# Optimization experiments

Measured on AMD Instinct MI355X. Metric: run time of the kernel, lower is better.

The kernel has to match this reference:

```python
import jax, jax.numpy as jnp
import numpy as np

# --- constants from init_kwargs / module defaults ---
H, W, C = 720, 1280, 2
T_EVT, T_PROP = 10, 10
T_TOTAL = T_EVT + T_PROP          # 20 temporal steps (10 event + 10 propagation)
TAU, THR0 = 10.0, 1.0             # LIF time constant, base threshold
ALPHA, TARGET_RATE = 0.1, 0.1     # PENT adaptation
THR_MIN, THR_MAX = 0.1, 10.0
N_EVENTS = 4_000_000


def setup_inputs() -> dict:
    key = jax.random.key(0)
    k1, k2, k3, k4 = jax.random.split(key, 4)
    x = jax.random.randint(k1, (N_EVENTS,), 0, W, dtype=jnp.int32)
    y = jax.random.randint(k2, (N_EVENTS,), 0, H, dtype=jnp.int32)
    p = jax.random.randint(k3, (N_EVENTS,), 0, 2, dtype=jnp.int32)
    t = jax.random.uniform(k4, (N_EVENTS,), dtype=jnp.float32)
    return {"x": x, "y": y, "p": p, "t": t}


def _build_buffer(x, y, p, t):
    # TemporalBuffer.forward: bin events into first T_EVT steps, rest are zeros.
    tmin, tmax = t.min(), t.max()
    denom = jnp.where(tmax > tmin, tmax - tmin, jnp.float32(1.0))
    t_norm = jnp.where(tmax > tmin, (t - tmin) / denom * (T_EVT - 1e-6), 0.0)
    t_idx = jnp.clip(t_norm.astype(jnp.int32), 0, T_EVT - 1)
    xi = jnp.clip(x, 0, W - 1)
    yi = jnp.clip(y, 0, H - 1)
    c_idx = p  # p in {0,1} -> channel index directly (p.min() >= 0 branch)
    buf = jnp.zeros((T_TOTAL, C, H, W), jnp.float32)
    return buf.at[t_idx, c_idx, yi, xi].add(1.0)


def reference(x, y, p, t):
    buffer = _build_buffer(x, y, p, t)  # (T, C, H, W)
    decay = jnp.float32(np.exp(-1.0 / TAU))

    def step(carry, frame):
        mem, thr = carry
        # LIFBuffer: decay + accumulate
        mem = mem * decay + frame
        spk = (mem >= thr).astype(jnp.float32)
        mem = mem - spk * thr  # soft ('subtract') reset
        # AdaptiveThreshold (PENT): homeostatic rate-based adaptation
        rate = spk.mean()
        thr = jnp.clip(thr + ALPHA * (rate - TARGET_RATE), THR_MIN, THR_MAX)
        return (mem, thr), spk

    mem0 = jnp.zeros((C, H, W), jnp.float32)
    (_, _), spikes = jax.lax.scan(step, (mem0, jnp.float32(THR0)), buffer)
    return spikes  # (T, C, H, W) binary spike activity maps
```

## Files before the change

kernel.cpp:

```cpp
#include <hip/hip_runtime.h>
#include <cstddef>

#define HH 720
#define WW 1280
#define FRAME 1843200
#define FRAME4 460800
#define T_EVT 10
#define T_TOTAL 20
#define ARRIVE64 (1ULL << 32)

#define ONBLK 256
#define ONTHR 1024
#define ONWPB 16
#define ONT (ONBLK * ONTHR)

#define SBLK 1024
#define STHR 256
#define SWPB 4
#define PIXB 1800
#define NGROUP4 450
#define HIST_W 9000
#define RBLK 512
#define RTHR 1024
#define NBUCKET 1024

#define MAT_OFF   0u
#define CS_OFF    (512u * 1024u * 4u)
#define SB_OFF    (CS_OFF + 4096u)
#define KEY_OFF   (SB_OFF + 8192u)
#define SEG_OFF(n) (KEY_OFF + 4u * (unsigned)(n))
#define WS_NEED(n) ((size_t)SEG_OFF(n) + 2ull * (size_t)(n) + 256ull)

__device__ unsigned g_minkey;
__device__ unsigned g_maxkey;
__device__ unsigned long long g_grp[T_TOTAL][16][16];
__device__ unsigned long long g_top[T_TOTAL][16];
__device__ unsigned g_rel[T_TOTAL][32];
__device__ unsigned long long g_n1[T_TOTAL][64][16];
__device__ unsigned long long g_n2[T_TOTAL][4][16];
__device__ unsigned long long g_n3[T_TOTAL][16];
__device__ unsigned g_relg[T_TOTAL][64][32];

__device__ __forceinline__ unsigned f2key(float f) {
    unsigned b = __float_as_uint(f);
    return b ^ ((unsigned)(((int)b) >> 31) | 0x80000000u);
}
__device__ __forceinline__ float key2f(unsigned k) {
    unsigned b = (k & 0x80000000u) ? (k ^ 0x80000000u) : ~k;
    return __uint_as_float(b);
}

__device__ __forceinline__ int event_bin_t(float tv, float tmin, float tmax) {
#pragma clang fp contract(off)
    float tn;
    if (tmax > tmin) tn = (tv - tmin) / (tmax - tmin) * (float)(10.0 - 1e-6);
    else tn = 0.0f;
    int ti = (int)tn;
    return ti < 0 ? 0 : (ti > T_EVT - 1 ? T_EVT - 1 : ti);
}
__device__ __forceinline__ int event_pixel(int xi, int yi, int ci) {
    xi = xi < 0 ? 0 : (xi > WW - 1 ? WW - 1 : xi);
    yi = yi < 0 ? 0 : (yi > HH - 1 ? HH - 1 : yi);
    return ci * (HH * WW) + yi * WW + xi;
}

__global__ void init_kernel() {
    const int gtid = blockIdx.x * blockDim.x + threadIdx.x;
    const int gs = gridDim.x * blockDim.x;
    if (gtid == 0) { g_minkey = 0xFFFFFFFFu; g_maxkey = 0u; }
    unsigned long long* a = &g_grp[0][0][0];
    for (int i = gtid; i < T_TOTAL * 16 * 16; i += gs) a[i] = 0ull;
    unsigned long long* b = &g_top[0][0];
    for (int i = gtid; i < T_TOTAL * 16; i += gs) b[i] = 0ull;
    unsigned* c = &g_rel[0][0];
    for (int i = gtid; i < T_TOTAL * 32; i += gs) c[i] = 0u;
    unsigned long long* d = &g_n1[0][0][0];
    for (int i = gtid; i < T_TOTAL * 64 * 16; i += gs) d[i] = 0ull;
    unsigned long long* e = &g_n2[0][0][0];
    for (int i = gtid; i < T_TOTAL * 4 * 16; i += gs) e[i] = 0ull;
    unsigned long long* f = &g_n3[0][0];
    for (int i = gtid; i < T_TOTAL * 16; i += gs) f[i] = 0ull;
    unsigned* g = &g_relg[0][0][0];
    for (int i = gtid; i < T_TOTAL * 64 * 32; i += gs) g[i] = 0u;
}

__device__ __forceinline__ void minmax_body(const float* __restrict__ t, int n,
                                            int gtid, int gstride) {
    unsigned mn = 0xFFFFFFFFu, mx = 0u;
    const int n4 = n >> 2;
    const float4* t4 = (const float4*)t;
    for (int i = gtid; i < n4; i += gstride) {
        float4 tv = t4[i];
        unsigned k0 = f2key(tv.x), k1 = f2key(tv.y);
        unsigned k2 = f2key(tv.z), k3 = f2key(tv.w);
        unsigned a = k0 < k1 ? k0 : k1, b = k2 < k3 ? k2 : k3;
        unsigned c = a < b ? a : b;
        mn = mn < c ? mn : c;
        a = k0 > k1 ? k0 : k1; b = k2 > k3 ? k2 : k3;
        c = a > b ? a : b;
        mx = mx > c ? mx : c;
    }
    for (int i = (n4 << 2) + gtid; i < n; i += gstride) {
        unsigned k = f2key(t[i]);
        mn = mn < k ? mn : k;
        mx = mx > k ? mx : k;
    }
    for (int off = 32; off > 0; off >>= 1) {
        unsigned omn = (unsigned)__shfl_down((int)mn, off, 64);
        unsigned omx = (unsigned)__shfl_down((int)mx, off, 64);
        mn = mn < omn ? mn : omn;
        mx = mx > omx ? mx : omx;
    }
    __shared__ unsigned smn[16], smx[16];
    int lane = threadIdx.x & 63, wv = threadIdx.x >> 6;
    if (lane == 0) { smn[wv] = mn; smx[wv] = mx; }
    __syncthreads();
    if (threadIdx.x == 0) {
        int nw = blockDim.x >> 6;
        for (int i = 1; i < nw; ++i) {
            mn = mn < smn[i] ? mn : smn[i];
            mx = mx > smx[i] ? mx : smx[i];
        }
        atomicMin(&g_minkey, mn);
        atomicMax(&g_maxkey, mx);
    }
}

__global__ void minmax_kernel(const float* __restrict__ t, int n) {
    minmax_body(t, n, blockIdx.x * blockDim.x + threadIdx.x,
                gridDim.x * blockDim.x);
}

__global__ void minmax_zero_kernel(const float* __restrict__ t, int n,
                                   uint4* __restrict__ hist16v) {
    const int gtid = blockIdx.x * blockDim.x + threadIdx.x;
    const int gstride = gridDim.x * blockDim.x;
    const uint4 z = make_uint4(0u, 0u, 0u, 0u);
    const int nz = T_EVT * FRAME / 8;
    for (int i = gtid; i < nz; i += gstride) hist16v[i] = z;
    minmax_body(t, n, gtid, gstride);
}

__global__ __launch_bounds__(RTHR) void passA_kernel(
        const int* __restrict__ x, const int* __restrict__ y,
        const int* __restrict__ p, const float* __restrict__ t,
        unsigned* __restrict__ mat, unsigned* __restrict__ keys, int n) {
    __shared__ unsigned cnt[NBUCKET];
    for (int i = threadIdx.x; i < NBUCKET; i += blockDim.x) cnt[i] = 0u;
    __syncthreads();
    const float tmin = key2f(g_minkey);
    const float tmax = key2f(g_maxkey);
    const int chunk = (n + (int)gridDim.x - 1) / (int)gridDim.x;
    const int s0 = blockIdx.x * chunk;
    const int s1 = min(n, s0 + chunk);
    for (int i = s0 + threadIdx.x; i < s1; i += blockDim.x) {
        int pix = event_pixel(x[i], y[i], p[i]);
        int ti = event_bin_t(t[i], tmin, tmax);
        keys[i] = ((unsigned)ti << 21) | (unsigned)pix;
        atomicAdd(&cnt[pix / PIXB], 1u);
    }
    __syncthreads();
    for (int i = threadIdx.x; i < NBUCKET; i += blockDim.x)
        mat[blockIdx.x * NBUCKET + i] = cnt[i];
}

__global__ void offsets_col_kernel(unsigned* __restrict__ mat,
                                   unsigned* __restrict__ colsum) {
    const int j = blockIdx.x;
    const int r = threadIdx.x;
    const int lane = r & 63, wv = r >> 6;
    unsigned v = mat[r * NBUCKET + j];
    unsigned incl = v;
    for (int off = 1; off < 64; off <<= 1) {
        unsigned o = (unsigned)__shfl_up((int)incl, off, 64);
        if (lane >= off) incl += o;
    }
    __shared__ unsigned wtot[RBLK / 64];
    if (lane == 63) wtot[wv] = incl;
    __syncthreads();
    if (r == 0) {
        unsigned run = 0;
#pragma unroll
        for (int k = 0; k < RBLK / 64; ++k) { unsigned tmp = wtot[k]; wtot[k] = run; run += tmp; }
    }
    __syncthreads();
    unsigned ex = incl - v + wtot[wv];
    mat[r * NBUCKET + j] = ex;
    if (r == RBLK - 1) colsum[j] = ex + v;
}

__global__ void offsets_top_kernel(const unsigned* __restrict__ colsum,
                                   unsigned* __restrict__ seg_base) {
    const int j = threadIdx.x;
    const int lane = j & 63, wv = j >> 6;
    unsigned v = colsum[j];
    unsigned incl = v;
    for (int off = 1; off < 64; off <<= 1) {
        unsigned o = (unsigned)__shfl_up((int)incl, off, 64);
        if (lane >= off) incl += o;
    }
    __shared__ unsigned wtot[16];
    if (lane == 63) wtot[wv] = incl;
    __syncthreads();
    if (j == 0) {
        unsigned run = 0;
#pragma unroll
        for (int k = 0; k < 16; ++k) { unsigned tmp = wtot[k]; wtot[k] = run; run += tmp; }
    }
    __syncthreads();
    unsigned ex = incl - v + wtot[wv];
    seg_base[j] = ex;
    if (j == NBUCKET - 1) seg_base[NBUCKET] = ex + v;
}

__global__ __launch_bounds__(RTHR) void passB_kernel(
        const unsigned* __restrict__ keys, const unsigned* __restrict__ mat,
        const unsigned* __restrict__ seg_base,
        unsigned short* __restrict__ seg, int n) {
    __shared__ unsigned base[NBUCKET];
    for (int i = threadIdx.x; i < NBUCKET; i += blockDim.x)
        base[i] = mat[blockIdx.x * NBUCKET + i] + seg_base[i];
    __syncthreads();
    const int chunk = (n + (int)gridDim.x - 1) / (int)gridDim.x;
    const int s0 = blockIdx.x * chunk;
    const int s1 = min(n, s0 + chunk);
    for (int i = s0 + threadIdx.x; i < s1; i += blockDim.x) {
        unsigned k = keys[i];
        int pix = (int)(k & 0x1FFFFFu);
        int ti = (int)(k >> 21);
        int bkt = pix / PIXB;
        int lb = ti * PIXB + (pix - bkt * PIXB);
        unsigned idx = atomicAdd(&base[bkt], 1u);
        seg[idx] = (unsigned short)lb;
    }
}

__global__ __launch_bounds__(STHR, 4) void scan_new(float* __restrict__ out,
                                                    const unsigned short* __restrict__ seg,
                                                    const unsigned* __restrict__ seg_base) {
#pragma clang fp contract(off)
    const float decay = (float)0.9048374180359595;
    const int tid = threadIdx.x;
    const int lane = tid & 63;
    const int b = blockIdx.x;
    const int pix0 = b * PIXB;

    __shared__ unsigned lds_hist[HIST_W];
    __shared__ unsigned lds_arr[T_TOTAL];
    __shared__ unsigned lds_tot[T_TOTAL];

    for (int i = tid; i < HIST_W; i += STHR) lds_hist[i] = 0u;
    if (tid < T_TOTAL) { lds_arr[tid] = 0u; lds_tot[tid] = 0u; }
    __syncthreads();

    {
        const int e0 = (int)seg_base[b];
        const int e1 = (int)seg_base[b + 1];
        for (int i = e0 + tid; i < e1; i += STHR) {
            unsigned lb = seg[i];
            atomicAdd(&lds_hist[lb >> 1], 1u << ((lb & 1u) << 4));
        }
    }
    __syncthreads();

    const bool has1 = tid < (NGROUP4 - STHR);
    float4 mem0 = make_float4(0.f, 0.f, 0.f, 0.f);
    float4 mem1 = make_float4(0.f, 0.f, 0.f, 0.f);
    float thr = 1.0f;

    for (int s = 0; s < T_TOTAL; ++s) {
        float* ob = out + (size_t)s * FRAME + pix0;
        int cnt = 0;

        {
            float4 f;
            if (s < T_EVT) {
                int w = s * 900 + (tid << 1);
                unsigned w0 = lds_hist[w], w1 = lds_hist[w + 1];
                f = make_float4((float)(w0 & 0xFFFFu), (float)(w0 >> 16),
                                (float)(w1 & 0xFFFFu), (float)(w1 >> 16));
            } else f = make_float4(0.f, 0.f, 0.f, 0.f);
            float4 m, spk;
            m.x = mem0.x * decay; m.x = m.x + f.x;
            m.y = mem0.y * decay; m.y = m.y + f.y;
            m.z = mem0.z * decay; m.z = m.z + f.z;
            m.w = mem0.w * decay; m.w = m.w + f.w;
            spk.x = (m.x >= thr) ? 1.0f : 0.0f;
            spk.y = (m.y >= thr) ? 1.0f : 0.0f;
            spk.z = (m.z >= thr) ? 1.0f : 0.0f;
            spk.w = (m.w >= thr) ? 1.0f : 0.0f;
            ((float4*)ob)[tid] = spk;
            mem0.x = m.x - spk.x * thr;
            mem0.y = m.y - spk.y * thr;
            mem0.z = m.z - spk.z * thr;
            mem0.w = m.w - spk.w * thr;
            cnt += (int)spk.x + (int)spk.y + (int)spk.z + (int)spk.w;
        }
        if (has1) {
            int g = tid + STHR;
            float4 f;
            if (s < T_EVT) {
                int w = s * 900 + (g << 1);
                unsigned w0 = lds_hist[w], w1 = lds_hist[w + 1];
                f = make_float4((float)(w0 & 0xFFFFu), (float)(w0 >> 16),
                                (float)(w1 & 0xFFFFu), (float)(w1 >> 16));
            } else f = make_float4(0.f, 0.f, 0.f, 0.f);
            float4 m, spk;
            m.x = mem1.x * decay; m.x = m.x + f.x;
            m.y = mem1.y * decay; m.y = m.y + f.y;
            m.z = mem1.z * decay; m.z = m.z + f.z;
            m.w = mem1.w * decay; m.w = m.w + f.w;
            spk.x = (m.x >= thr) ? 1.0f : 0.0f;
            spk.y = (m.y >= thr) ? 1.0f : 0.0f;
            spk.z = (m.z >= thr) ? 1.0f : 0.0f;
            spk.w = (m.w >= thr) ? 1.0f : 0.0f;
            ((float4*)ob)[g] = spk;
            mem1.x = m.x - spk.x * thr;
            mem1.y = m.y - spk.y * thr;
            mem1.z = m.z - spk.z * thr;
            mem1.w = m.w - spk.w * thr;
            cnt += (int)spk.x + (int)spk.y + (int)spk.z + (int)spk.w;
        }

        if (s == T_TOTAL - 1) break;

        for (int off = 32; off > 0; off >>= 1) cnt += __shfl_down(cnt, off, 64);
        unsigned total;
        if (lane == 0) {
            unsigned old = __hip_atomic_fetch_add(&lds_arr[s],
                               (unsigned)cnt + (1u << 16),
                               __ATOMIC_RELAXED, __HIP_MEMORY_SCOPE_WORKGROUP);
            if ((old >> 16) == SWPB - 1) {
                unsigned bc = (old + (unsigned)cnt) & 0xFFFFu;
                const int g1 = b >> 4;
                unsigned long long a1 = __hip_atomic_fetch_add(
                    &g_n1[s][g1][0], (unsigned long long)bc + ARRIVE64,
                    __ATOMIC_RELAXED, __HIP_MEMORY_SCOPE_AGENT);
                if ((unsigned)(a1 >> 32) == 15u) {
                    unsigned c1 = (unsigned)a1 + bc;
                    const int g2 = g1 >> 4;
                    unsigned long long a2 = __hip_atomic_fetch_add(
                        &g_n2[s][g2][0], (unsigned long long)c1 + ARRIVE64,
                        __ATOMIC_RELAXED, __HIP_MEMORY_SCOPE_AGENT);
                    if ((unsigned)(a2 >> 32) == 15u) {
                        unsigned c2 = (unsigned)a2 + c1;
                        unsigned long long a3 = __hip_atomic_fetch_add(
                            &g_n3[s][0], (unsigned long long)c2 + ARRIVE64,
                            __ATOMIC_RELAXED, __HIP_MEMORY_SCOPE_AGENT);
                        if ((unsigned)(a3 >> 32) == 3u) {
                            unsigned tot = (unsigned)a3 + c2;
                            for (int g = 0; g < 64; ++g)
                                __hip_atomic_store(&g_relg[s][g][0], tot + 1u,
                                    __ATOMIC_RELAXED, __HIP_MEMORY_SCOPE_AGENT);
                        }
                    }
                }
                unsigned f;
                do {
                    __builtin_amdgcn_s_sleep(1);
                    f = __hip_atomic_load(&g_relg[s][g1][0], __ATOMIC_RELAXED,
                                          __HIP_MEMORY_SCOPE_AGENT);
                } while (f == 0u);
                total = f - 1u;
                __hip_atomic_store(&lds_tot[s], f,
                                   __ATOMIC_RELAXED, __HIP_MEMORY_SCOPE_WORKGROUP);
            } else {
                unsigned f;
                do {
                    __builtin_amdgcn_s_sleep(1);
                    f = __hip_atomic_load(&lds_tot[s], __ATOMIC_RELAXED,
                                          __HIP_MEMORY_SCOPE_WORKGROUP);
                } while (f == 0u);
                total = f - 1u;
            }
        }
        total = (unsigned)__shfl((int)total, 0, 64);
        float rate = (float)total / 1843200.0f;
        thr = thr + 0.1f * (rate - 0.1f);
        thr = fminf(fmaxf(thr, 0.1f), 10.0f);
    }
}

__global__ void scatter_kernel(const int* __restrict__ x, const int* __restrict__ y,
                               const int* __restrict__ p, const float* __restrict__ t,
                               unsigned* __restrict__ hist32, int n) {
    int i = blockIdx.x * blockDim.x + threadIdx.x;
    if (i >= n) return;
    float tmin = key2f(g_minkey);
    float tmax = key2f(g_maxkey);
    int ti = event_bin_t(t[i], tmin, tmax);
    int pix = event_pixel(x[i], y[i], p[i]);
    size_t bidx = (size_t)ti * FRAME + pix;
    atomicAdd(hist32 + (bidx >> 1), 1u << ((bidx & 1) << 4));
}

__global__ __launch_bounds__(ONTHR) void scan_old(float* __restrict__ out) {
#pragma clang fp contract(off)
    const float decay = (float)0.9048374180359595;
    const int gtid = blockIdx.x * ONTHR + threadIdx.x;
    const int lane = threadIdx.x & 63;
    const uint2 uz2 = make_uint2(0u, 0u);
    float4 mem0 = make_float4(0.f, 0.f, 0.f, 0.f);
    float4 mem1 = make_float4(0.f, 0.f, 0.f, 0.f);
    const bool has1 = (gtid + ONT) < FRAME4;
    float thr = 1.0f;
    const uint2* hist2 = (const uint2*)(out + (size_t)T_EVT * FRAME);
    __shared__ unsigned lds_arr[T_TOTAL];
    __shared__ unsigned lds_tot[T_TOTAL];
    if (threadIdx.x < T_TOTAL) { lds_arr[threadIdx.x] = 0u; lds_tot[threadIdx.x] = 0u; }
    __syncthreads();
    uint2 u0 = hist2[gtid];
    uint2 u1 = has1 ? hist2[gtid + ONT] : uz2;
    for (int s = 0; s < T_TOTAL; ++s) {
        float4* o4 = (float4*)(out + (size_t)s * FRAME);
        int cnt = 0;
        {
            float4 m, spk;
            m.x = mem0.x * decay; m.x = m.x + (float)(u0.x & 0xFFFFu);
            m.y = mem0.y * decay; m.y = m.y + (float)(u0.x >> 16);
            m.z = mem0.z * decay; m.z = m.z + (float)(u0.y & 0xFFFFu);
            m.w = mem0.w * decay; m.w = m.w + (float)(u0.y >> 16);
            spk.x = (m.x >= thr) ? 1.0f : 0.0f;
            spk.y = (m.y >= thr) ? 1.0f : 0.0f;
            spk.z = (m.z >= thr) ? 1.0f : 0.0f;
            spk.w = (m.w >= thr) ? 1.0f : 0.0f;
            o4[gtid] = spk;
            mem0.x = m.x - spk.x * thr; mem0.y = m.y - spk.y * thr;
            mem0.z = m.z - spk.z * thr; mem0.w = m.w - spk.w * thr;
            cnt += (int)spk.x + (int)spk.y + (int)spk.z + (int)spk.w;
        }
        if (has1) {
            float4 m, spk;
            m.x = mem1.x * decay; m.x = m.x + (float)(u1.x & 0xFFFFu);
            m.y = mem1.y * decay; m.y = m.y + (float)(u1.x >> 16);
            m.z = mem1.z * decay; m.z = m.z + (float)(u1.y & 0xFFFFu);
            m.w = mem1.w * decay; m.w = m.w + (float)(u1.y >> 16);
            spk.x = (m.x >= thr) ? 1.0f : 0.0f;
            spk.y = (m.y >= thr) ? 1.0f : 0.0f;
            spk.z = (m.z >= thr) ? 1.0f : 0.0f;
            spk.w = (m.w >= thr) ? 1.0f : 0.0f;
            o4[gtid + ONT] = spk;
            mem1.x = m.x - spk.x * thr; mem1.y = m.y - spk.y * thr;
            mem1.z = m.z - spk.z * thr; mem1.w = m.w - spk.w * thr;
            cnt += (int)spk.x + (int)spk.y + (int)spk.z + (int)spk.w;
        }
        if (s + 1 < T_EVT) {
            const uint2* hn = hist2 + (size_t)(s + 1) * FRAME4;
            u0 = hn[gtid];
            u1 = has1 ? hn[gtid + ONT] : uz2;
        } else { u0 = uz2; u1 = uz2; }
        if (s == T_TOTAL - 1) break;
        for (int off = 32; off > 0; off >>= 1) cnt += __shfl_down(cnt, off, 64);
        unsigned total;
        if (lane == 0) {
            unsigned old = __hip_atomic_fetch_add(&lds_arr[s],
                               (unsigned)cnt + (1u << 16),
                               __ATOMIC_RELAXED, __HIP_MEMORY_SCOPE_WORKGROUP);
            if ((old >> 16) == ONWPB - 1) {
                unsigned bc = (old + (unsigned)cnt) & 0xFFFFu;
                const int gid = blockIdx.x >> 4;
                unsigned long long gold = __hip_atomic_fetch_add(
                    &g_grp[s][gid][0], (unsigned long long)bc + ARRIVE64,
                    __ATOMIC_RELAXED, __HIP_MEMORY_SCOPE_AGENT);
                if ((unsigned)(gold >> 32) == 15u) {
                    unsigned gc = (unsigned)gold + bc;
                    unsigned long long told = __hip_atomic_fetch_add(
                        &g_top[s][0], (unsigned long long)gc + ARRIVE64,
                        __ATOMIC_RELAXED, __HIP_MEMORY_SCOPE_AGENT);
                    if ((unsigned)(told >> 32) == 15u) {
                        unsigned tot = (unsigned)told + gc;
                        __hip_atomic_store(&g_rel[s][0], tot + 1u,
                                           __ATOMIC_RELAXED, __HIP_MEMORY_SCOPE_AGENT);
                    }
                }
                unsigned f;
                do {
                    __builtin_amdgcn_s_sleep(1);
                    f = __hip_atomic_load(&g_rel[s][0], __ATOMIC_RELAXED,
                                          __HIP_MEMORY_SCOPE_AGENT);
                } while (f == 0u);
                total = f - 1u;
                __hip_atomic_store(&lds_tot[s], f,
                                   __ATOMIC_RELAXED, __HIP_MEMORY_SCOPE_WORKGROUP);
            } else {
                unsigned f;
                do {
                    __builtin_amdgcn_s_sleep(1);
                    f = __hip_atomic_load(&lds_tot[s], __ATOMIC_RELAXED,
                                          __HIP_MEMORY_SCOPE_WORKGROUP);
                } while (f == 0u);
                total = f - 1u;
            }
        }
        total = (unsigned)__shfl((int)total, 0, 64);
        float rate = (float)total / 1843200.0f;
        thr = thr + 0.1f * (rate - 0.1f);
        thr = fminf(fmaxf(thr, 0.1f), 10.0f);
    }
}

extern "C" void kernel_launch(void* const* d_in, const int* in_sizes, int n_in,
                              void* d_out, int out_size, void* d_ws, size_t ws_size,
                              hipStream_t stream) {
    const int*   x = (const int*)d_in[0];
    const int*   y = (const int*)d_in[1];
    const int*   p = (const int*)d_in[2];
    const float* t = (const float*)d_in[3];
    float* out = (float*)d_out;
    const int n = in_sizes[0];

    init_kernel<<<64, 256, 0, stream>>>();

    if (d_ws != nullptr && ws_size >= WS_NEED(n)) {
        unsigned* mat = (unsigned*)((char*)d_ws + MAT_OFF);
        unsigned* colsum = (unsigned*)((char*)d_ws + CS_OFF);
        unsigned* seg_base = (unsigned*)((char*)d_ws + SB_OFF);
        unsigned* keys = (unsigned*)((char*)d_ws + KEY_OFF);
        unsigned short* seg = (unsigned short*)((char*)d_ws + SEG_OFF(n));

        minmax_kernel<<<1024, 256, 0, stream>>>(t, n);
        passA_kernel<<<RBLK, RTHR, 0, stream>>>(x, y, p, t, mat, keys, n);
        offsets_col_kernel<<<NBUCKET, RBLK, 0, stream>>>(mat, colsum);
        offsets_top_kernel<<<1, NBUCKET, 0, stream>>>(colsum, seg_base);
        passB_kernel<<<RBLK, RTHR, 0, stream>>>(keys, mat, seg_base, seg, n);

        dim3 g(SBLK), b(STHR);
        void* args[] = { (void*)&out, (void*)&seg, (void*)&seg_base };
        hipLaunchCooperativeKernel((void*)scan_new, g, b, args, 0, stream);
    } else {
        unsigned* hist32 = (unsigned*)(out + (size_t)T_EVT * FRAME);
        minmax_zero_kernel<<<1024, 256, 0, stream>>>(t, n, (uint4*)hist32);
        scatter_kernel<<<(n + 255) / 256, 256, 0, stream>>>(x, y, p, t, hist32, n);
        dim3 g(ONBLK), b(ONTHR);
        void* args[] = { (void*)&out };
        hipLaunchCooperativeKernel((void*)scan_old, g, b, args, 0, stream);
    }
}
```

Before: 366.5 us.

## Fuse minmax into counting pass, merge offset kernels, drop intermediate key buffer

Min/max reduction of t is folded into the bucket-counting pass, since counting only needs pixel coordinates. The two offset-scan kernels become one, using a last-block-done atomic counter for the top-level scan. The 4-byte-per-event keys array is removed, and passB recomputes pixel and time bin directly from x, y, p and t. This cuts two kernel launches and one write-plus-read of a 16 MB key buffer, at the cost of rereading the input arrays in passB.

```diff
diff --git a/kernel.cpp b/kernel.cpp
--- a/kernel.cpp
+++ b/kernel.cpp
@@ -22,17 +22,18 @@
 #define HIST_W 9000
 #define RBLK 512
 #define RTHR 1024
+#define OTHR 512
 #define NBUCKET 1024
 
 #define MAT_OFF   0u
 #define CS_OFF    (512u * 1024u * 4u)
 #define SB_OFF    (CS_OFF + 4096u)
-#define KEY_OFF   (SB_OFF + 8192u)
-#define SEG_OFF(n) (KEY_OFF + 4u * (unsigned)(n))
-#define WS_NEED(n) ((size_t)SEG_OFF(n) + 2ull * (size_t)(n) + 256ull)
+#define SEG_OFF   (SB_OFF + 8192u)
+#define WS_NEED(n) ((size_t)SEG_OFF + 2ull * (size_t)(n) + 256ull)
 
 __device__ unsigned g_minkey;
 __device__ unsigned g_maxkey;
+__device__ unsigned g_done;
 __device__ unsigned long long g_grp[T_TOTAL][16][16];
 __device__ unsigned long long g_top[T_TOTAL][16];
 __device__ unsigned g_rel[T_TOTAL][32];
@@ -67,7 +68,7 @@
 __global__ void init_kernel() {
     const int gtid = blockIdx.x * blockDim.x + threadIdx.x;
     const int gs = gridDim.x * blockDim.x;
-    if (gtid == 0) { g_minkey = 0xFFFFFFFFu; g_maxkey = 0u; }
+    if (gtid == 0) { g_minkey = 0xFFFFFFFFu; g_maxkey = 0u; g_done = 0u; }
     unsigned long long* a = &g_grp[0][0][0];
     for (int i = gtid; i < T_TOTAL * 16 * 16; i += gs) a[i] = 0ull;
     unsigned long long* b = &g_top[0][0];
@@ -126,11 +127,6 @@
     }
 }
 
-__global__ void minmax_kernel(const float* __restrict__ t, int n) {
-    minmax_body(t, n, blockIdx.x * blockDim.x + threadIdx.x,
-                gridDim.x * blockDim.x);
-}
-
 __global__ void minmax_zero_kernel(const float* __restrict__ t, int n,
                                    uint4* __restrict__ hist16v) {
     const int gtid = blockIdx.x * blockDim.x + threadIdx.x;
@@ -141,12 +137,99 @@
     minmax_body(t, n, gtid, gstride);
 }
 
-__global__ __launch_bounds__(RTHR) void passA_kernel(
+__global__ __launch_bounds__(RTHR) void count_minmax_kernel(
         const int* __restrict__ x, const int* __restrict__ y,
         const int* __restrict__ p, const float* __restrict__ t,
-        unsigned* __restrict__ mat, unsigned* __restrict__ keys, int n) {
+        unsigned* __restrict__ mat, int n) {
     __shared__ unsigned cnt[NBUCKET];
     for (int i = threadIdx.x; i < NBUCKET; i += blockDim.x) cnt[i] = 0u;
+    __syncthreads();
+    const int chunk = (n + (int)gridDim.x - 1) / (int)gridDim.x;
+    const int s0 = blockIdx.x * chunk;
+    const int s1 = min(n, s0 + chunk);
+    for (int i = s0 + threadIdx.x; i < s1; i += blockDim.x) {
+        int pix = event_pixel(x[i], y[i], p[i]);
+        atomicAdd(&cnt[pix / PIXB], 1u);
+    }
+    minmax_body(t, n, blockIdx.x * blockDim.x + threadIdx.x,
+                gridDim.x * blockDim.x);
+    __syncthreads();
+    for (int i = threadIdx.x; i < NBUCKET; i += blockDim.x)
+        mat[blockIdx.x * NBUCKET + i] = cnt[i];
+}
+
+__global__ __launch_bounds__(OTHR) void offsets_kernel(
+        unsigned* __restrict__ mat, unsigned* __restrict__ colsum,
+        unsigned* __restrict__ seg_base) {
+    const int j = blockIdx.x;
+    const int r = threadIdx.x;
+    const int lane = r & 63, wv = r >> 6;
+    __shared__ unsigned wtot[OTHR / 64];
+    __shared__ unsigned last_flag;
+    {
+        unsigned v = mat[r * NBUCKET + j];
+        unsigned incl = v;
+        for (int off = 1; off < 64; off <<= 1) {
+            unsigned o = (unsigned)__shfl_up((int)incl, off, 64);
+            if (lane >= off) incl += o;
+        }
+        if (lane == 63) wtot[wv] = incl;
+        __syncthreads();
+        if (r == 0) {
+            unsigned run = 0;
+#pragma unroll
+            for (int k = 0; k < OTHR / 64; ++k) { unsigned tmp = wtot[k]; wtot[k] = run; run += tmp; }
+        }
+        __syncthreads();
+        unsigned ex = incl - v + wtot[wv];
+        mat[r * NBUCKET + j] = ex;
+        if (r == OTHR - 1) colsum[j] = ex + v;
+    }
+    __syncthreads();
+    if (r == 0) {
+        __threadfence();
+        unsigned old = __hip_atomic_fetch_add(&g_done, 1u, __ATOMIC_RELAXED,
+                                              __HIP_MEMORY_SCOPE_AGENT);
+        last_flag = (old == NBUCKET - 1) ? 1u : 0u;
+    }
+    __syncthreads();
+    if (last_flag) {
+        __shared__ unsigned sb[NBUCKET];
+        __shared__ unsigned wt2[OTHR / 64];
+        for (int i = r; i < NBUCKET; i += OTHR)
+            sb[i] = __hip_atomic_load(&colsum[i], __ATOMIC_RELAXED,
+                                      __HIP_MEMORY_SCOPE_AGENT);
+        __syncthreads();
+        unsigned a = sb[2 * r], bb = sb[2 * r + 1];
+        unsigned s = a + bb;
+        unsigned incl = s;
+        for (int off = 1; off < 64; off <<= 1) {
+            unsigned o = (unsigned)__shfl_up((int)incl, off, 64);
+            if (lane >= off) incl += o;
+        }
+        if (lane == 63) wt2[wv] = incl;
+        __syncthreads();
+        if (r == 0) {
+            unsigned run = 0;
+#pragma unroll
+            for (int k = 0; k < OTHR / 64; ++k) { unsigned tmp = wt2[k]; wt2[k] = run; run += tmp; }
+        }
+        __syncthreads();
+        unsigned exs = incl - s + wt2[wv];
+        seg_base[2 * r] = exs;
+        seg_base[2 * r + 1] = exs + a;
+        if (r == OTHR - 1) seg_base[NBUCKET] = exs + s;
+    }
+}
+
+__global__ __launch_bounds__(RTHR) void passB_kernel(
+        const int* __restrict__ x, const int* __restrict__ y,
+        const int* __restrict__ p, const float* __restrict__ t,
+        const unsigned* __restrict__ mat, const unsigned* __restrict__ seg_base,
+        unsigned short* __restrict__ seg, int n) {
+    __shared__ unsigned base[NBUCKET];
+    for (int i = threadIdx.x; i < NBUCKET; i += blockDim.x)
+        base[i] = mat[blockIdx.x * NBUCKET + i] + seg_base[i];
     __syncthreads();
     const float tmin = key2f(g_minkey);
     const float tmax = key2f(g_maxkey);
@@ -156,78 +239,6 @@
     for (int i = s0 + threadIdx.x; i < s1; i += blockDim.x) {
         int pix = event_pixel(x[i], y[i], p[i]);
         int ti = event_bin_t(t[i], tmin, tmax);
-        keys[i] = ((unsigned)ti << 21) | (unsigned)pix;
-        atomicAdd(&cnt[pix / PIXB], 1u);
-    }
-    __syncthreads();
-    for (int i = threadIdx.x; i < NBUCKET; i += blockDim.x)
-        mat[blockIdx.x * NBUCKET + i] = cnt[i];
-}
-
-__global__ void offsets_col_kernel(unsigned* __restrict__ mat,
-                                   unsigned* __restrict__ colsum) {
-    const int j = blockIdx.x;
-    const int r = threadIdx.x;
-    const int lane = r & 63, wv = r >> 6;
-    unsigned v = mat[r * NBUCKET + j];
-    unsigned incl = v;
-    for (int off = 1; off < 64; off <<= 1) {
-        unsigned o = (unsigned)__shfl_up((int)incl, off, 64);
-        if (lane >= off) incl += o;
-    }
-    __shared__ unsigned wtot[RBLK / 64];
-    if (lane == 63) wtot[wv] = incl;
-    __syncthreads();
-    if (r == 0) {
-        unsigned run = 0;
-#pragma unroll
-        for (int k = 0; k < RBLK / 64; ++k) { unsigned tmp = wtot[k]; wtot[k] = run; run += tmp; }
-    }
-    __syncthreads();
-    unsigned ex = incl - v + wtot[wv];
-    mat[r * NBUCKET + j] = ex;
-    if (r == RBLK - 1) colsum[j] = ex + v;
-}
-
-__global__ void offsets_top_kernel(const unsigned* __restrict__ colsum,
-                                   unsigned* __restrict__ seg_base) {
-    const int j = threadIdx.x;
-    const int lane = j & 63, wv = j >> 6;
-    unsigned v = colsum[j];
-    unsigned incl = v;
-    for (int off = 1; off < 64; off <<= 1) {
-        unsigned o = (unsigned)__shfl_up((int)incl, off, 64);
-        if (lane >= off) incl += o;
-    }
-    __shared__ unsigned wtot[16];
-    if (lane == 63) wtot[wv] = incl;
-    __syncthreads();
-    if (j == 0) {
-        unsigned run = 0;
-#pragma unroll
-        for (int k = 0; k < 16; ++k) { unsigned tmp = wtot[k]; wtot[k] = run; run += tmp; }
-    }
-    __syncthreads();
-    unsigned ex = incl - v + wtot[wv];
-    seg_base[j] = ex;
-    if (j == NBUCKET - 1) seg_base[NBUCKET] = ex + v;
-}
-
-__global__ __launch_bounds__(RTHR) void passB_kernel(
-        const unsigned* __restrict__ keys, const unsigned* __restrict__ mat,
-        const unsigned* __restrict__ seg_base,
-        unsigned short* __restrict__ seg, int n) {
-    __shared__ unsigned base[NBUCKET];
-    for (int i = threadIdx.x; i < NBUCKET; i += blockDim.x)
-        base[i] = mat[blockIdx.x * NBUCKET + i] + seg_base[i];
-    __syncthreads();
-    const int chunk = (n + (int)gridDim.x - 1) / (int)gridDim.x;
-    const int s0 = blockIdx.x * chunk;
-    const int s1 = min(n, s0 + chunk);
-    for (int i = s0 + threadIdx.x; i < s1; i += blockDim.x) {
-        unsigned k = keys[i];
-        int pix = (int)(k & 0x1FFFFFu);
-        int ti = (int)(k >> 21);
         int bkt = pix / PIXB;
         int lb = ti * PIXB + (pix - bkt * PIXB);
         unsigned idx = atomicAdd(&base[bkt], 1u);
@@ -515,14 +526,11 @@
         unsigned* mat = (unsigned*)((char*)d_ws + MAT_OFF);
         unsigned* colsum = (unsigned*)((char*)d_ws + CS_OFF);
         unsigned* seg_base = (unsigned*)((char*)d_ws + SB_OFF);
-        unsigned* keys = (unsigned*)((char*)d_ws + KEY_OFF);
-        unsigned short* seg = (unsigned short*)((char*)d_ws + SEG_OFF(n));
-
-        minmax_kernel<<<1024, 256, 0, stream>>>(t, n);
-        passA_kernel<<<RBLK, RTHR, 0, stream>>>(x, y, p, t, mat, keys, n);
-        offsets_col_kernel<<<NBUCKET, RBLK, 0, stream>>>(mat, colsum);
-        offsets_top_kernel<<<1, NBUCKET, 0, stream>>>(colsum, seg_base);
-        passB_kernel<<<RBLK, RTHR, 0, stream>>>(keys, mat, seg_base, seg, n);
+        unsigned short* seg = (unsigned short*)((char*)d_ws + SEG_OFF);
+
+        count_minmax_kernel<<<RBLK, RTHR, 0, stream>>>(x, y, p, t, mat, n);
+        offsets_kernel<<<NBUCKET, OTHR, 0, stream>>>(mat, colsum, seg_base);
+        passB_kernel<<<RBLK, RTHR, 0, stream>>>(x, y, p, t, mat, seg_base, seg, n);
 
         dim3 g(SBLK), b(STHR);
         void* args[] = { (void*)&out, (void*)&seg, (void*)&seg_base };
```

Result: slower. 394.2 us (+7.6%).

## Fuse minmax into passA, top-level offset scan into passB, defer time binning

Applied to the files above, without the earlier changes.

Removes the standalone minmax kernel by computing the time min/max inside passA, which now stores only the pixel index in keys. The time bin is computed in passB, which rereads t once the global min/max are ready. The 1024-bucket top-level exclusive scan is folded into every passB block, and block 0 writes seg_base for the scan kernel. This drops two kernel launches and their serialization at the cost of rereading t in passB and a redundant small scan in each block.

```diff
diff --git a/kernel.cpp b/kernel.cpp
--- a/kernel.cpp
+++ b/kernel.cpp
@@ -22,6 +22,7 @@
 #define HIST_W 9000
 #define RBLK 512
 #define RTHR 1024
+#define OTHR 512
 #define NBUCKET 1024
 
 #define MAT_OFF   0u
@@ -126,11 +127,6 @@
     }
 }
 
-__global__ void minmax_kernel(const float* __restrict__ t, int n) {
-    minmax_body(t, n, blockIdx.x * blockDim.x + threadIdx.x,
-                gridDim.x * blockDim.x);
-}
-
 __global__ void minmax_zero_kernel(const float* __restrict__ t, int n,
                                    uint4* __restrict__ hist16v) {
     const int gtid = blockIdx.x * blockDim.x + threadIdx.x;
@@ -148,24 +144,23 @@
     __shared__ unsigned cnt[NBUCKET];
     for (int i = threadIdx.x; i < NBUCKET; i += blockDim.x) cnt[i] = 0u;
     __syncthreads();
-    const float tmin = key2f(g_minkey);
-    const float tmax = key2f(g_maxkey);
     const int chunk = (n + (int)gridDim.x - 1) / (int)gridDim.x;
     const int s0 = blockIdx.x * chunk;
     const int s1 = min(n, s0 + chunk);
     for (int i = s0 + threadIdx.x; i < s1; i += blockDim.x) {
         int pix = event_pixel(x[i], y[i], p[i]);
-        int ti = event_bin_t(t[i], tmin, tmax);
-        keys[i] = ((unsigned)ti << 21) | (unsigned)pix;
+        keys[i] = (unsigned)pix;
         atomicAdd(&cnt[pix / PIXB], 1u);
     }
+    minmax_body(t, n, blockIdx.x * blockDim.x + threadIdx.x,
+                gridDim.x * blockDim.x);
     __syncthreads();
     for (int i = threadIdx.x; i < NBUCKET; i += blockDim.x)
         mat[blockIdx.x * NBUCKET + i] = cnt[i];
 }
 
-__global__ void offsets_col_kernel(unsigned* __restrict__ mat,
-                                   unsigned* __restrict__ colsum) {
+__global__ __launch_bounds__(OTHR) void offsets_col_kernel(
+        unsigned* __restrict__ mat, unsigned* __restrict__ colsum) {
     const int j = blockIdx.x;
     const int r = threadIdx.x;
     const int lane = r & 63, wv = r >> 6;
@@ -175,59 +170,60 @@
         unsigned o = (unsigned)__shfl_up((int)incl, off, 64);
         if (lane >= off) incl += o;
     }
-    __shared__ unsigned wtot[RBLK / 64];
+    __shared__ unsigned wtot[OTHR / 64];
     if (lane == 63) wtot[wv] = incl;
     __syncthreads();
     if (r == 0) {
         unsigned run = 0;
 #pragma unroll
-        for (int k = 0; k < RBLK / 64; ++k) { unsigned tmp = wtot[k]; wtot[k] = run; run += tmp; }
+        for (int k = 0; k < OTHR / 64; ++k) { unsigned tmp = wtot[k]; wtot[k] = run; run += tmp; }
     }
     __syncthreads();
     unsigned ex = incl - v + wtot[wv];
     mat[r * NBUCKET + j] = ex;
-    if (r == RBLK - 1) colsum[j] = ex + v;
-}
-
-__global__ void offsets_top_kernel(const unsigned* __restrict__ colsum,
-                                   unsigned* __restrict__ seg_base) {
-    const int j = threadIdx.x;
-    const int lane = j & 63, wv = j >> 6;
-    unsigned v = colsum[j];
-    unsigned incl = v;
-    for (int off = 1; off < 64; off <<= 1) {
-        unsigned o = (unsigned)__shfl_up((int)incl, off, 64);
-        if (lane >= off) incl += o;
-    }
-    __shared__ unsigned wtot[16];
-    if (lane == 63) wtot[wv] = incl;
-    __syncthreads();
-    if (j == 0) {
-        unsigned run = 0;
-#pragma unroll
-        for (int k = 0; k < 16; ++k) { unsigned tmp = wtot[k]; wtot[k] = run; run += tmp; }
-    }
-    __syncthreads();
-    unsigned ex = incl - v + wtot[wv];
-    seg_base[j] = ex;
-    if (j == NBUCKET - 1) seg_base[NBUCKET] = ex + v;
+    if (r == OTHR - 1) colsum[j] = ex + v;
 }
 
 __global__ __launch_bounds__(RTHR) void passB_kernel(
-        const unsigned* __restrict__ keys, const unsigned* __restrict__ mat,
-        const unsigned* __restrict__ seg_base,
+        const unsigned* __restrict__ keys, const float* __restrict__ t,
+        const unsigned* __restrict__ mat, const unsigned* __restrict__ colsum,
+        unsigned* __restrict__ seg_base_out,
         unsigned short* __restrict__ seg, int n) {
     __shared__ unsigned base[NBUCKET];
-    for (int i = threadIdx.x; i < NBUCKET; i += blockDim.x)
-        base[i] = mat[blockIdx.x * NBUCKET + i] + seg_base[i];
-    __syncthreads();
+    __shared__ unsigned wt2[RTHR / 64];
+    {
+        const int j = threadIdx.x;
+        const int lane = j & 63, wv = j >> 6;
+        unsigned v = colsum[j];
+        unsigned incl = v;
+        for (int off = 1; off < 64; off <<= 1) {
+            unsigned o = (unsigned)__shfl_up((int)incl, off, 64);
+            if (lane >= off) incl += o;
+        }
+        if (lane == 63) wt2[wv] = incl;
+        __syncthreads();
+        if (j == 0) {
+            unsigned run = 0;
+#pragma unroll
+            for (int k = 0; k < RTHR / 64; ++k) { unsigned tmp = wt2[k]; wt2[k] = run; run += tmp; }
+        }
+        __syncthreads();
+        unsigned ex = incl - v + wt2[wv];
+        base[j] = mat[blockIdx.x * NBUCKET + j] + ex;
+        if (blockIdx.x == 0) {
+            seg_base_out[j] = ex;
+            if (j == NBUCKET - 1) seg_base_out[NBUCKET] = ex + v;
+        }
+    }
+    __syncthreads();
+    const float tmin = key2f(g_minkey);
+    const float tmax = key2f(g_maxkey);
     const int chunk = (n + (int)gridDim.x - 1) / (int)gridDim.x;
     const int s0 = blockIdx.x * chunk;
     const int s1 = min(n, s0 + chunk);
     for (int i = s0 + threadIdx.x; i < s1; i += blockDim.x) {
-        unsigned k = keys[i];
-        int pix = (int)(k & 0x1FFFFFu);
-        int ti = (int)(k >> 21);
+        int pix = (int)keys[i];
+        int ti = event_bin_t(t[i], tmin, tmax);
         int bkt = pix / PIXB;
         int lb = ti * PIXB + (pix - bkt * PIXB);
         unsigned idx = atomicAdd(&base[bkt], 1u);
@@ -518,11 +514,9 @@
         unsigned* keys = (unsigned*)((char*)d_ws + KEY_OFF);
         unsigned short* seg = (unsigned short*)((char*)d_ws + SEG_OFF(n));
 
-        minmax_kernel<<<1024, 256, 0, stream>>>(t, n);
         passA_kernel<<<RBLK, RTHR, 0, stream>>>(x, y, p, t, mat, keys, n);
-        offsets_col_kernel<<<NBUCKET, RBLK, 0, stream>>>(mat, colsum);
-        offsets_top_kernel<<<1, NBUCKET, 0, stream>>>(colsum, seg_base);
-        passB_kernel<<<RBLK, RTHR, 0, stream>>>(keys, mat, seg_base, seg, n);
+        offsets_col_kernel<<<NBUCKET, OTHR, 0, stream>>>(mat, colsum);
+        passB_kernel<<<RBLK, RTHR, 0, stream>>>(keys, t, mat, colsum, seg_base, seg, n);
 
         dim3 g(SBLK), b(STHR);
         void* args[] = { (void*)&out, (void*)&seg, (void*)&seg_base };
```

Result: faster. 349.5 us (-4.6%).
